# Kernel tuning notes

Measured on AMD Instinct MI355X. Metric: run time of the kernel, lower is better.

## Reference

```python
import jax, jax.numpy as jnp
import numpy as np

H = 64  # hidden_dimension
F = 8   # number_of_input_features
P = 64  # prediction_length
B = 1024
T = 512


def _lstm_cell(x, h, c, Wih, Whh, bih, bhh):
    # PyTorch gate order: input, forget, cell(g), output
    gates = x @ Wih.T + h @ Whh.T + (bih + bhh)  # [B, 4H]
    i, f, g, o = jnp.split(gates, 4, axis=-1)
    c_new = jax.nn.sigmoid(f) * c + jax.nn.sigmoid(i) * jnp.tanh(g)
    h_new = jax.nn.sigmoid(o) * jnp.tanh(c_new)
    return h_new, c_new


def setup_inputs() -> dict:
    key = jax.random.key(0)
    ks = jax.random.split(key, 11)
    s = 1.0 / np.sqrt(H)
    u = lambda k, shape: jax.random.uniform(k, shape, jnp.float32, -s, s)
    return {
        "input_sequence": jax.random.normal(ks[0], (B, T, F), jnp.float32),
        "enc_Wih": u(ks[1], (4 * H, F)),
        "enc_Whh": u(ks[2], (4 * H, H)),
        "enc_bih": u(ks[3], (4 * H,)),
        "enc_bhh": u(ks[4], (4 * H,)),
        "dec_Wih": u(ks[5], (4 * H, F)),
        "dec_Whh": u(ks[6], (4 * H, H)),
        "dec_bih": u(ks[7], (4 * H,)),
        "dec_bhh": u(ks[8], (4 * H,)),
        "fc_W": u(ks[9], (F, H)),
        "fc_b": u(ks[10], (F,)),
    }


def reference(input_sequence, enc_Wih, enc_Whh, enc_bih, enc_bhh,
              dec_Wih, dec_Whh, dec_bih, dec_bhh, fc_W, fc_b):
    Bn = input_sequence.shape[0]
    h0 = jnp.zeros((Bn, H), input_sequence.dtype)
    c0 = jnp.zeros((Bn, H), input_sequence.dtype)

    # ---- Encoder: scan over time ----
    xs = jnp.swapaxes(input_sequence, 0, 1)  # [T, B, F]

    def enc_step(carry, x_t):
        h, c = carry
        h, c = _lstm_cell(x_t, h, c, enc_Wih, enc_Whh, enc_bih, enc_bhh)
        return (h, c), None

    (h, c), _ = jax.lax.scan(enc_step, (h0, c0), xs)

    x_last = input_sequence[:, -1, :]  # [B, F]

    def dec_step(carry, _):
        h, c, x = carry
        h, c = _lstm_cell(x, h, c, dec_Wih, dec_Whh, dec_bih, dec_bhh)
        pred = h @ fc_W.T + fc_b  # [B, F]
        return (h, c, pred), pred

    _, preds = jax.lax.scan(dec_step, (h, c, x_last), None, length=P)
    return jnp.swapaxes(preds, 0, 1)  # [B, P, F]
```

## Files before the change

kernel.cpp:

```cpp
#include <hip/hip_runtime.h>


#define Hh 64
#define Ff 8
#define Tt 512
#define Pp 64
#define BATCH 1024
#define MB 4
#define NBLK (BATCH / MB)
#define ROWS 72
#define ABUF (16 * ROWS + 64)
#define XSTRIDE 32

typedef __attribute__((ext_vector_type(8))) _Float16 half8;
typedef __attribute__((ext_vector_type(4))) _Float16 half4;
typedef __attribute__((ext_vector_type(4))) float f32x4;

#define LOG2E  1.44269504088896340736f
#define K2LOG2 2.88538008177792681472f

__device__ __forceinline__ float rcp_(float x)  { return __builtin_amdgcn_rcpf(x); }
__device__ __forceinline__ float exp2_(float x) { return __builtin_amdgcn_exp2f(x); }
__device__ __forceinline__ int arow_base(int m) { return m * ROWS + (m & 3) * 16; }

__device__ __forceinline__ void load_wfrags(
    const float* __restrict__ Whh, const float* __restrict__ Wih,
    int wv, int q, int col, half8 w0[4], half8 w1[4], half8 wx[4])
{
    #pragma unroll
    for (int Tg = 0; Tg < 4; ++Tg) {
        int g = Tg * 64 + wv * 16 + col;
        float sc = (Tg == 2) ? K2LOG2 : LOG2E;
        const float* r0 = Whh + g * 64 + q * 8;
        #pragma unroll
        for (int j = 0; j < 8; ++j) {
            w0[Tg][j] = (_Float16)(r0[j] * sc);
            w1[Tg][j] = (_Float16)(r0[32 + j] * sc);
            wx[Tg][j] = (q == 0) ? (_Float16)(Wih[g * 8 + j] * sc) : (_Float16)0.f;
        }
    }
}

__device__ __forceinline__ void pchain(half8 ax, const half8 wx[4],
                                       const f32x4 biasv[4], f32x4 P[4])
{
    P[2] = __builtin_amdgcn_mfma_f32_16x16x32_f16(ax, wx[2], biasv[2], 0, 0, 0);
    P[0] = __builtin_amdgcn_mfma_f32_16x16x32_f16(ax, wx[0], biasv[0], 0, 0, 0);
    P[1] = __builtin_amdgcn_mfma_f32_16x16x32_f16(ax, wx[1], biasv[1], 0, 0, 0);
    P[3] = __builtin_amdgcn_mfma_f32_16x16x32_f16(ax, wx[3], biasv[3], 0, 0, 0);
}

__device__ __forceinline__ float qcell(half8 a0, half8 a1,
    const half8 w0[4], const half8 w1[4], const f32x4 P[4], float& cS)
{
    f32x4 Qg = __builtin_amdgcn_mfma_f32_16x16x32_f16(a0, w0[2], P[2], 0, 0, 0);
    f32x4 Qi = __builtin_amdgcn_mfma_f32_16x16x32_f16(a0, w0[0], P[0], 0, 0, 0);
    f32x4 Qf = __builtin_amdgcn_mfma_f32_16x16x32_f16(a0, w0[1], P[1], 0, 0, 0);
    f32x4 Qo = __builtin_amdgcn_mfma_f32_16x16x32_f16(a0, w0[3], P[3], 0, 0, 0);
    Qg = __builtin_amdgcn_mfma_f32_16x16x32_f16(a1, w1[2], Qg, 0, 0, 0);
    Qi = __builtin_amdgcn_mfma_f32_16x16x32_f16(a1, w1[0], Qi, 0, 0, 0);
    Qf = __builtin_amdgcn_mfma_f32_16x16x32_f16(a1, w1[1], Qf, 0, 0, 0);
    Qo = __builtin_amdgcn_mfma_f32_16x16x32_f16(a1, w1[3], Qo, 0, 0, 0);

    float eg = exp2_(Qg[0]);
    float ei = exp2_(-Qi[0]);
    float ef = exp2_(-Qf[0]);
    float eo = exp2_(-Qo[0]);
    float it = (eg - 1.f) * rcp_((1.f + ei) * (1.f + eg));
    float sf = rcp_(1.f + ef);
    cS = __builtin_fmaf(sf, cS, K2LOG2 * it);
    float cc = fminf(fmaxf(cS, -60.f), 60.f);
    float ec = exp2_(cc);
    return (ec - 1.f) * rcp_((1.f + eo) * (1.f + ec));
}

__global__ __launch_bounds__(256, 1)
void seq2seq_v11(const float* __restrict__ x_seq,
                 const float* __restrict__ eWih, const float* __restrict__ eWhh,
                 const float* __restrict__ ebih, const float* __restrict__ ebhh,
                 const float* __restrict__ dWih, const float* __restrict__ dWhh,
                 const float* __restrict__ dbih, const float* __restrict__ dbhh,
                 const float* __restrict__ fcW,  const float* __restrict__ fcb,
                 float* __restrict__ out)
{
    __shared__ __align__(16) _Float16 xs[(Tt + 2) * XSTRIDE];
    __shared__ __align__(16) _Float16 A0[ABUF];
    __shared__ __align__(16) _Float16 A1[ABUF];
    __shared__ float fcWT[Hh * 9 + 8];
    __shared__ float sfcb[Ff];
    __shared__ __align__(16) _Float16 xdec[MB * Ff];

    const int tid  = threadIdx.x;
    const int wv   = tid >> 6;
    const int lane = tid & 63;
    const int q    = lane >> 4;
    const int col  = lane & 15;
    const int u    = wv * 16 + col;
    const int b0   = blockIdx.x * MB;

    half8 w0[4], w1[4], wx[4];
    load_wfrags(eWhh, eWih, wv, q, col, w0, w1, wx);
    f32x4 biasv[4];
    #pragma unroll
    for (int Tg = 0; Tg < 4; ++Tg) {
        int g = Tg * 64 + u;
        float sc = (Tg == 2) ? K2LOG2 : LOG2E;
        float bv = (ebih[g] + ebhh[g]) * sc;
        biasv[Tg] = (f32x4){bv, bv, bv, bv};
    }

    { int* Z0 = (int*)A0; int* Z1 = (int*)A1;
      for (int i = tid; i < ABUF / 2; i += 256) { Z0[i] = 0; Z1[i] = 0; } }
    for (int i = tid; i < Ff * Hh; i += 256) { int f = i >> 6, uu = i & 63; fcWT[uu * 9 + f] = fcW[i]; }
    if (tid < Ff) sfcb[tid] = fcb[tid];
    if (tid < 32) ((int*)xs)[Tt * 16 + tid] = 0;
    for (int i = tid; i < MB * Tt * 2; i += 256) {
        int b   = i >> 10;
        int rem = i & 1023;
        int t   = rem >> 1;
        int f4  = (rem & 1) * 4;
        const float* src = x_seq + ((size_t)(b0 + b) * Tt + t) * Ff + f4;
        half4 s = { (_Float16)src[0], (_Float16)src[1], (_Float16)src[2], (_Float16)src[3] };
        *(half4*)(&xs[t * XSTRIDE + b * 8 + f4]) = s;
    }
    __syncthreads();

    const _Float16* arA = A0 + arow_base(col) + q * 8;
    const _Float16* arB = A1 + arow_base(col) + q * 8;
    _Float16* hwA = A0 + 4 * q * ROWS + u;
    _Float16* hwB = A1 + 4 * q * ROWS + u;
    const _Float16* xq = xs + (col >> 2) * 8;

    float cS = 0.f;
    f32x4 P[4];
    {   half8 ax = *(const half8*)(xq);
        pchain(ax, wx, biasv, P);
        xq += XSTRIDE; }

    for (int t = 0; t < Tt; t += 2) {
        __syncthreads();
        {
            half8 ax = *(const half8*)(xq); xq += XSTRIDE;
            half8 a0 = *(const half8*)(arA);
            half8 a1 = *(const half8*)(arA + 32);
            float hn = qcell(a0, a1, w0, w1, P, cS);
            *hwB = (_Float16)hn;
            pchain(ax, wx, biasv, P);
        }
        __syncthreads();
        {
            half8 ax = *(const half8*)(xq); xq += XSTRIDE;
            half8 a0 = *(const half8*)(arB);
            half8 a1 = *(const half8*)(arB + 32);
            float hn = qcell(a0, a1, w0, w1, P, cS);
            *hwA = (_Float16)hn;
            pchain(ax, wx, biasv, P);
        }
    }

    load_wfrags(dWhh, dWih, wv, q, col, w0, w1, wx);
    #pragma unroll
    for (int Tg = 0; Tg < 4; ++Tg) {
        int g = Tg * 64 + u;
        float sc = (Tg == 2) ? K2LOG2 : LOG2E;
        float bv = (dbih[g] + dbhh[g]) * sc;
        biasv[Tg] = (f32x4){bv, bv, bv, bv};
    }
    if (tid < MB * Ff) xdec[tid] = xs[(Tt - 1) * XSTRIDE + tid];
    __syncthreads();

    float* predbuf = (float*)xs;
    const _Float16* xdp = xdec + (col >> 2) * 8;

    for (int p = 0; p < Pp; ++p) {
        const _Float16* ar = (p & 1) ? arB : arA;
        _Float16*       hw = (p & 1) ? hwA : hwB;
        const _Float16* hb = (p & 1) ? A0  : A1;
        half8 ax = *(const half8*)(xdp);
        pchain(ax, wx, biasv, P);
        half8 a0 = *(const half8*)(ar);
        half8 a1 = *(const half8*)(ar + 32);
        float hn = qcell(a0, a1, w0, w1, P, cS);
        *hw = (_Float16)hn;
        __syncthreads();
        if (tid < MB * Ff) {
            int b = tid >> 3, f = tid & 7;
            const _Float16* hr = hb + (4 * b) * ROWS;
            float s = sfcb[f];
            #pragma unroll
            for (int ch = 0; ch < 8; ++ch) {
                half8 hh = *(const half8*)(hr + ch * 8);
                #pragma unroll
                for (int j = 0; j < 8; ++j)
                    s += (float)hh[j] * fcWT[(ch * 8 + j) * 9 + f];
            }
            predbuf[b * (Pp * Ff) + p * Ff + f] = s;
            xdec[tid] = (_Float16)s;
        }
        __syncthreads();
    }

    {
        f32x4* out4 = (f32x4*)out + (size_t)b0 * (Pp * Ff / 4);
        const f32x4* pb4 = (const f32x4*)predbuf;
        for (int i = tid; i < MB * Pp * Ff / 4; i += 256)
            out4[i] = pb4[i];
    }
}

extern "C" void kernel_launch(void* const* d_in, const int* in_sizes, int n_in,
                              void* d_out, int out_size, void* d_ws, size_t ws_size,
                              hipStream_t stream) {
    (void)in_sizes; (void)n_in; (void)d_ws; (void)ws_size; (void)out_size;
    hipLaunchKernelGGL(seq2seq_v11, dim3(NBLK), dim3(256), 0, stream,
                       (const float*)d_in[0],
                       (const float*)d_in[1], (const float*)d_in[2],
                       (const float*)d_in[3], (const float*)d_in[4],
                       (const float*)d_in[5], (const float*)d_in[6],
                       (const float*)d_in[7], (const float*)d_in[8],
                       (const float*)d_in[9], (const float*)d_in[10],
                       (float*)d_out);
}
```

Before: 261.1 us.

## Fold decoder FC feedback into recurrent weights and compute predictions via MFMA

Algebraically folds the autoregressive feedback (pred = fcW·h + fcb fed back through dWih) into fused recurrent weights Whh + Wih·fcW and a fused bias, so decoder steps after the first need no separate input chain and only one barrier per step. The FC projection is done with two MFMAs per step from the already-loaded h fragments, replacing the scalar 32-thread dot product and its extra sync. Precomputing the fused weights in fp16 changes rounding, since the fed-back prediction is no longer quantised separately. The decoder is a small share of total steps next to the 512 encoder steps.

```diff
diff --git a/kernel.cpp b/kernel.cpp
--- a/kernel.cpp
+++ b/kernel.cpp
@@ -75,7 +75,7 @@
 }
 
 __global__ __launch_bounds__(256, 1)
-void seq2seq_v11(const float* __restrict__ x_seq,
+void seq2seq_v12(const float* __restrict__ x_seq,
                  const float* __restrict__ eWih, const float* __restrict__ eWhh,
                  const float* __restrict__ ebih, const float* __restrict__ ebhh,
                  const float* __restrict__ dWih, const float* __restrict__ dWhh,
@@ -86,9 +86,6 @@
     __shared__ __align__(16) _Float16 xs[(Tt + 2) * XSTRIDE];
     __shared__ __align__(16) _Float16 A0[ABUF];
     __shared__ __align__(16) _Float16 A1[ABUF];
-    __shared__ float fcWT[Hh * 9 + 8];
-    __shared__ float sfcb[Ff];
-    __shared__ __align__(16) _Float16 xdec[MB * Ff];
 
     const int tid  = threadIdx.x;
     const int wv   = tid >> 6;
@@ -111,8 +108,6 @@
 
     { int* Z0 = (int*)A0; int* Z1 = (int*)A1;
       for (int i = tid; i < ABUF / 2; i += 256) { Z0[i] = 0; Z1[i] = 0; } }
-    for (int i = tid; i < Ff * Hh; i += 256) { int f = i >> 6, uu = i & 63; fcWT[uu * 9 + f] = fcW[i]; }
-    if (tid < Ff) sfcb[tid] = fcb[tid];
     if (tid < 32) ((int*)xs)[Tt * 16 + tid] = 0;
     for (int i = tid; i < MB * Tt * 2; i += 256) {
         int b   = i >> 10;
@@ -158,47 +153,85 @@
         }
     }
 
-    load_wfrags(dWhh, dWih, wv, q, col, w0, w1, wx);
+    half8 axl = *(const half8*)(xs + (Tt - 1) * XSTRIDE + (col >> 2) * 8);
+
+    half8 wp0[4], wp1[4];
+    f32x4 biasp[4];
     #pragma unroll
     for (int Tg = 0; Tg < 4; ++Tg) {
         int g = Tg * 64 + u;
         float sc = (Tg == 2) ? K2LOG2 : LOG2E;
-        float bv = (dbih[g] + dbhh[g]) * sc;
-        biasv[Tg] = (f32x4){bv, bv, bv, bv};
-    }
-    if (tid < MB * Ff) xdec[tid] = xs[(Tt - 1) * XSTRIDE + tid];
-    __syncthreads();
+        #pragma unroll
+        for (int j = 0; j < 8; ++j) {
+            int k0 = q * 8 + j;
+            float v0 = dWhh[g * 64 + k0];
+            float v1 = dWhh[g * 64 + 32 + k0];
+            w0[Tg][j] = (_Float16)(v0 * sc);
+            w1[Tg][j] = (_Float16)(v1 * sc);
+            wx[Tg][j] = (q == 0) ? (_Float16)(dWih[g * 8 + j] * sc) : (_Float16)0.f;
+            float s0 = v0, s1 = v1;
+            #pragma unroll
+            for (int f = 0; f < 8; ++f) {
+                float wif = dWih[g * 8 + f];
+                s0 = __builtin_fmaf(wif, fcW[f * 64 + k0], s0);
+                s1 = __builtin_fmaf(wif, fcW[f * 64 + 32 + k0], s1);
+            }
+            wp0[Tg][j] = (_Float16)(s0 * sc);
+            wp1[Tg][j] = (_Float16)(s1 * sc);
+        }
+        float bb = dbih[g] + dbhh[g];
+        float bp = bb;
+        #pragma unroll
+        for (int f = 0; f < 8; ++f) bp = __builtin_fmaf(dWih[g * 8 + f], fcb[f], bp);
+        biasv[Tg] = (f32x4){bb * sc, bb * sc, bb * sc, bb * sc};
+        biasp[Tg] = (f32x4){bp * sc, bp * sc, bp * sc, bp * sc};
+    }
+    half8 wf0, wf1;
+    f32x4 biasf;
+    {
+        #pragma unroll
+        for (int j = 0; j < 8; ++j) {
+            wf0[j] = (col < 8) ? (_Float16)fcW[col * 64 + q * 8 + j]      : (_Float16)0.f;
+            wf1[j] = (col < 8) ? (_Float16)fcW[col * 64 + 32 + q * 8 + j] : (_Float16)0.f;
+        }
+        float fb = (col < 8) ? fcb[col] : 0.f;
+        biasf = (f32x4){fb, fb, fb, fb};
+    }
 
     float* predbuf = (float*)xs;
-    const _Float16* xdp = xdec + (col >> 2) * 8;
-
-    for (int p = 0; p < Pp; ++p) {
+    const bool pw = (wv == 0) && (col < 8);
+
+    __syncthreads();
+    {
+        half8 a0 = *(const half8*)(arA);
+        half8 a1 = *(const half8*)(arA + 32);
+        pchain(axl, wx, biasv, P);
+        float hn = qcell(a0, a1, w0, w1, P, cS);
+        *hwB = (_Float16)hn;
+    }
+
+    for (int p = 1; p < Pp; ++p) {
+        __syncthreads();
         const _Float16* ar = (p & 1) ? arB : arA;
         _Float16*       hw = (p & 1) ? hwA : hwB;
-        const _Float16* hb = (p & 1) ? A0  : A1;
-        half8 ax = *(const half8*)(xdp);
-        pchain(ax, wx, biasv, P);
         half8 a0 = *(const half8*)(ar);
         half8 a1 = *(const half8*)(ar + 32);
-        float hn = qcell(a0, a1, w0, w1, P, cS);
+        float hn = qcell(a0, a1, wp0, wp1, biasp, cS);
         *hw = (_Float16)hn;
-        __syncthreads();
-        if (tid < MB * Ff) {
-            int b = tid >> 3, f = tid & 7;
-            const _Float16* hr = hb + (4 * b) * ROWS;
-            float s = sfcb[f];
-            #pragma unroll
-            for (int ch = 0; ch < 8; ++ch) {
-                half8 hh = *(const half8*)(hr + ch * 8);
-                #pragma unroll
-                for (int j = 0; j < 8; ++j)
-                    s += (float)hh[j] * fcWT[(ch * 8 + j) * 9 + f];
-            }
-            predbuf[b * (Pp * Ff) + p * Ff + f] = s;
-            xdec[tid] = (_Float16)s;
-        }
-        __syncthreads();
-    }
+        f32x4 F = __builtin_amdgcn_mfma_f32_16x16x32_f16(a0, wf0, biasf, 0, 0, 0);
+        F       = __builtin_amdgcn_mfma_f32_16x16x32_f16(a1, wf1, F,     0, 0, 0);
+        if (pw) predbuf[q * (Pp * Ff) + (p - 1) * Ff + col] = F[0];
+    }
+
+    __syncthreads();
+    {
+        half8 a0 = *(const half8*)(arA);
+        half8 a1 = *(const half8*)(arA + 32);
+        f32x4 F = __builtin_amdgcn_mfma_f32_16x16x32_f16(a0, wf0, biasf, 0, 0, 0);
+        F       = __builtin_amdgcn_mfma_f32_16x16x32_f16(a1, wf1, F,     0, 0, 0);
+        if (pw) predbuf[q * (Pp * Ff) + (Pp - 1) * Ff + col] = F[0];
+    }
+    __syncthreads();
 
     {
         f32x4* out4 = (f32x4*)out + (size_t)b0 * (Pp * Ff / 4);
@@ -212,7 +245,7 @@
                               void* d_out, int out_size, void* d_ws, size_t ws_size,
                               hipStream_t stream) {
     (void)in_sizes; (void)n_in; (void)d_ws; (void)ws_size; (void)out_size;
-    hipLaunchKernelGGL(seq2seq_v11, dim3(NBLK), dim3(256), 0, stream,
+    hipLaunchKernelGGL(seq2seq_v12, dim3(NBLK), dim3(256), 0, stream,
                        (const float*)d_in[0],
                        (const float*)d_in[1], (const float*)d_in[2],
                        (const float*)d_in[3], (const float*)d_in[4],
```

Result: faster. 219.8 us (-15.8%).
